# Performance work log

Measured on AMD Instinct MI355X. Metric: run time of the kernel, lower is better.

The kernel has to match this reference:

```python
import jax, jax.numpy as jnp
import numpy as np

B, N, D = 4, 1024, 1024
H = 16
DH = D // H  # 64
DROPOUT_P = 0.5


def setup_inputs() -> dict:
    key = jax.random.key(0)
    ks = jax.random.split(key, 6)
    query = jax.random.normal(ks[0], (B, N, D), dtype=jnp.float32)
    key_t = jax.random.normal(ks[1], (B, N, D), dtype=jnp.float32)
    value = jax.random.normal(ks[2], (B, N, D), dtype=jnp.float32)
    # torch Linear(D, 3D): weight [3D, D], bias [3D]
    W_qkv = jax.random.normal(ks[3], (3 * D, D), dtype=jnp.float32) * (1.0 / np.sqrt(D))
    b_qkv = jax.random.normal(ks[4], (3 * D,), dtype=jnp.float32) * 0.01
    # inverted dropout mask: keep_prob = 1 - p, kept entries scaled by 1/keep
    keep = 1.0 - DROPOUT_P
    drop_mask = (jax.random.uniform(ks[5], (B * H, N, N)) < keep).astype(jnp.float32) / keep
    return {"query": query, "key": key_t, "value": value,
            "W_qkv": W_qkv, "b_qkv": b_qkv, "drop_mask": drop_mask}


def _split_heads(t):
    # 'b n (h d) -> (b h) n d'
    b, n, _ = t.shape
    return t.reshape(b, n, H, DH).transpose(0, 2, 1, 3).reshape(b * H, n, DH)


def reference(query, key, value, W_qkv, b_qkv, drop_mask):
    # key/value args are unused by the original module (it derives q,k,v from query)
    qkv = query @ W_qkv.T + b_qkv                      # [b, n, 3d]
    q, k, v = jnp.split(qkv, 3, axis=-1)
    q, k, v = _split_heads(q), _split_heads(k), _split_heads(v)  # [(b h), n, dh]
    qk = jnp.einsum('znd,zmd->znm', q, k)              # [(b h), n, n]
    # faithful quirk: original does qk.div(1/sqrt(dh)) == qk * sqrt(dh)
    scaled_qk = qk * jnp.sqrt(jnp.float32(DH))
    attn = jax.nn.softmax(scaled_qk, axis=-1)
    attn = attn * drop_mask                            # deterministic inverted dropout
    out = jnp.einsum('znm,zmd->znd', attn, v)          # [(b h), n, dh]
    # '(b h) n d -> b n (h d)'
    out = out.reshape(B, H, N, DH).transpose(0, 2, 1, 3).reshape(B, N, D)
    return out
```

## Files before the change

kernel.cpp:

```cpp
#include <hip/hip_runtime.h>


typedef _Float16 f16;
typedef _Float16 f16x4 __attribute__((ext_vector_type(4)));
typedef _Float16 f16x8 __attribute__((ext_vector_type(8)));
typedef float    f32x4 __attribute__((ext_vector_type(4)));

#define MFMA16(a, b, c) __builtin_amdgcn_mfma_f32_16x16x32_f16((a), (b), (c), 0, 0, 0)

__device__ __forceinline__ void gll16(const f16* g, f16* l) {
  __builtin_amdgcn_global_load_lds(
      (const __attribute__((address_space(1))) unsigned int*)g,
      (__attribute__((address_space(3))) unsigned int*)l, 16, 0, 0);
}

__device__ __forceinline__ f16x8 ldsfrag(const f16* tile, int row, int chunk) {
  return *(const f16x8*)&tile[row * 64 + ((chunk ^ (row & 7)) << 3)];
}

__global__ __launch_bounds__(256) void cvt_split(const float4* __restrict__ s,
                                                 f16x4* __restrict__ hi,
                                                 f16x4* __restrict__ lo, int n4) {
  int i = blockIdx.x * 256 + threadIdx.x;
  if (i >= n4) return;
  float4 v = s[i];
  f16x4 h, l;
  h[0] = (f16)v.x; l[0] = (f16)(v.x - (float)h[0]);
  h[1] = (f16)v.y; l[1] = (f16)(v.y - (float)h[1]);
  h[2] = (f16)v.z; l[2] = (f16)(v.z - (float)h[2]);
  h[3] = (f16)v.w; l[3] = (f16)(v.w - (float)h[3]);
  hi[i] = h; lo[i] = l;
}

__global__ __launch_bounds__(256) void proj_gemm(
    const f16* __restrict__ qh, const f16* __restrict__ ql,
    const f16* __restrict__ wh, const f16* __restrict__ wl,
    const float* __restrict__ bias,
    f16* __restrict__ Qh, f16* __restrict__ Ql,
    f16* __restrict__ Kh, f16* __restrict__ Kl,
    f16* __restrict__ Vh) {
  __shared__ f16 As[128 * 32];
  __shared__ f16 Bs[128 * 32];
  const int tid = threadIdx.x;
  const int m0 = blockIdx.y * 128, n0 = blockIdx.x * 128;
  const int wid = tid >> 6, lane = tid & 63;
  const int wm = (wid >> 1) * 64, wn = (wid & 1) * 64;
  const int r16 = lane & 15, g = lane >> 4;

  f32x4 zero4 = {0.f, 0.f, 0.f, 0.f};
  f32x4 acc[4][4];
#pragma unroll
  for (int i = 0; i < 4; ++i)
#pragma unroll
    for (int j = 0; j < 4; ++j) acc[i][j] = zero4;

  const f16* At[3] = {qh, ql, qh};
  const f16* Bt[3] = {wh, wh, wl};
  const int nsteps = (n0 < 2048) ? 96 : 32;

  for (int s = 0; s < nsteps; ++s) {
    const int term = s >> 5, kk = (s & 31) << 5;
    const f16* Ab = At[term] + (size_t)m0 * 1024 + kk;
    const f16* Bb = Bt[term] + (size_t)n0 * 1024 + kk;
#pragma unroll
    for (int it = 0; it < 2; ++it) {
      int c = tid + it * 256;
      int row = c >> 2, cc = c & 3;
      gll16(Ab + row * 1024 + cc * 8, &As[c * 8]);
      gll16(Bb + row * 1024 + cc * 8, &Bs[c * 8]);
    }
    __syncthreads();
    f16x8 a[4], b[4];
#pragma unroll
    for (int i = 0; i < 4; ++i) {
      a[i] = *(const f16x8*)&As[(wm + i * 16 + r16) * 32 + g * 8];
      b[i] = *(const f16x8*)&Bs[(wn + i * 16 + r16) * 32 + g * 8];
    }
#pragma unroll
    for (int i = 0; i < 4; ++i)
#pragma unroll
      for (int j = 0; j < 4; ++j) acc[i][j] = MFMA16(a[i], b[j], acc[i][j]);
    __syncthreads();
  }

#pragma unroll
  for (int j = 0; j < 4; ++j) {
    const int col = n0 + wn + j * 16 + r16;
    const float bv = bias[col];
#pragma unroll
    for (int i = 0; i < 4; ++i) {
#pragma unroll
      for (int rr = 0; rr < 4; ++rr) {
        const int m = m0 + wm + i * 16 + g * 4 + rr;
        const float c = acc[i][j][rr] + bv;
        const int bi = m >> 10, n = m & 1023;
        if (col < 1024) {
          const int z = bi * 16 + (col >> 6), dh = col & 63;
          const size_t idx = ((size_t)z * 1024 + n) * 64 + dh;
          f16 h = (f16)c;
          Qh[idx] = h; Ql[idx] = (f16)(c - (float)h);
        } else if (col < 2048) {
          const int c2 = col - 1024;
          const int z = bi * 16 + (c2 >> 6), dh = c2 & 63;
          const size_t idx = ((size_t)z * 1024 + n) * 64 + dh;
          f16 h = (f16)c;
          Kh[idx] = h; Kl[idx] = (f16)(c - (float)h);
        } else {
          const int c2 = col - 2048;
          const int z = bi * 16 + (c2 >> 6), dh = c2 & 63;
          Vh[((size_t)z * 1024 + n) * 64 + dh] = (f16)c;
        }
      }
    }
  }
}

__global__ __launch_bounds__(256) void transp_v(const f16* __restrict__ Vh,
                                                f16* __restrict__ Vt) {
  __shared__ f16 t[64][80];
  const int z = blockIdx.y, nt = blockIdx.x;
  const int tid = threadIdx.x;
#pragma unroll
  for (int it = 0; it < 2; ++it) {
    int c = tid + it * 256;
    int row = c >> 3, cc = c & 7;
    *(f16x8*)&t[row][cc * 8] =
        *(const f16x8*)&Vh[(((size_t)z << 10) + nt * 64 + row) * 64 + cc * 8];
  }
  __syncthreads();
#pragma unroll
  for (int it = 0; it < 2; ++it) {
    int c = tid + it * 256;
    int dh = c >> 3, ncc = c & 7;
    f16x8 o;
#pragma unroll
    for (int j = 0; j < 8; ++j) o[j] = t[ncc * 8 + j][dh];
    *(f16x8*)&Vt[((size_t)z * 64 + dh) * 1024 + nt * 64 + ncc * 8] = o;
  }
}

__global__ __launch_bounds__(256) void attn(
    const f16* __restrict__ Qh_, const f16* __restrict__ Ql_,
    const f16* __restrict__ Kh_, const f16* __restrict__ Kl_,
    const f16* __restrict__ Vt_, const float* __restrict__ mask,
    float* __restrict__ out) {
  __shared__ f16 sm[5 * 4096];
  f16* Qhs = sm;
  f16* Qls = sm + 4096;
  f16* Khs = sm + 2 * 4096;
  f16* Kls = sm + 3 * 4096;
  f16* Vts = sm + 4 * 4096;
  f16* Ps = Khs;

  const int z = blockIdx.y, qt = blockIdx.x;
  const int q0 = qt * 64;
  const int tid = threadIdx.x, w = tid >> 6, lane = tid & 63;
  const int r16 = lane & 15, g = lane >> 4;

  const size_t qbase = ((size_t)z * 1024 + q0) * 64;
#pragma unroll
  for (int it = 0; it < 2; ++it) {
    int c = tid + it * 256;
    int row = c >> 3, p = c & 7, sc = p ^ (row & 7);
    gll16(Qh_ + qbase + row * 64 + sc * 8, &Qhs[c * 8]);
    gll16(Ql_ + qbase + row * 64 + sc * 8, &Qls[c * 8]);
  }
  __syncthreads();

  f16x8 qa[2], qla[2];
#pragma unroll
  for (int ks = 0; ks < 2; ++ks) {
    qa[ks] = ldsfrag(Qhs, w * 16 + r16, ks * 4 + g);
    qla[ks] = ldsfrag(Qls, w * 16 + r16, ks * 4 + g);
  }

  float mrow[4] = {-1e30f, -1e30f, -1e30f, -1e30f};
  float lrow[4] = {0.f, 0.f, 0.f, 0.f};
  f32x4 zero4 = {0.f, 0.f, 0.f, 0.f};
  f32x4 acc[4];
#pragma unroll
  for (int df = 0; df < 4; ++df) acc[df] = zero4;

  const float* mrow_base = mask + ((size_t)z << 20);

  for (int kt = 0; kt < 16; ++kt) {
    const int k0 = kt * 64;
    const size_t kbase = ((size_t)z * 1024 + k0) * 64;
    const size_t vbase = (size_t)z * 64 * 1024 + k0;
#pragma unroll
    for (int it = 0; it < 2; ++it) {
      int c = tid + it * 256;
      int row = c >> 3, p = c & 7, sc = p ^ (row & 7);
      gll16(Kh_ + kbase + row * 64 + sc * 8, &Khs[c * 8]);
      gll16(Kl_ + kbase + row * 64 + sc * 8, &Kls[c * 8]);
      gll16(Vt_ + vbase + (size_t)row * 1024 + sc * 8, &Vts[c * 8]);
    }
    __syncthreads();

    f32x4 s[4];
#pragma unroll
    for (int cf = 0; cf < 4; ++cf) {
      f32x4 t = zero4;
#pragma unroll
      for (int ks = 0; ks < 2; ++ks) {
        f16x8 kh = ldsfrag(Khs, cf * 16 + r16, ks * 4 + g);
        f16x8 kl = ldsfrag(Kls, cf * 16 + r16, ks * 4 + g);
        t = MFMA16(qa[ks], kh, t);
        t = MFMA16(qla[ks], kh, t);
        t = MFMA16(qa[ks], kl, t);
      }
      s[cf] = t;
    }

    float s8[4][4];
#pragma unroll
    for (int cf = 0; cf < 4; ++cf)
#pragma unroll
      for (int rr = 0; rr < 4; ++rr) s8[cf][rr] = s[cf][rr] * 8.0f;

    float rm[4];
#pragma unroll
    for (int rr = 0; rr < 4; ++rr)
      rm[rr] = fmaxf(fmaxf(s8[0][rr], s8[1][rr]), fmaxf(s8[2][rr], s8[3][rr]));
#pragma unroll
    for (int mk = 1; mk < 16; mk <<= 1)
#pragma unroll
      for (int rr = 0; rr < 4; ++rr)
        rm[rr] = fmaxf(rm[rr], __shfl_xor(rm[rr], mk, 64));

    float mnew[4], scal[4];
#pragma unroll
    for (int rr = 0; rr < 4; ++rr) {
      mnew[rr] = fmaxf(mrow[rr], rm[rr]);
      scal[rr] = __expf(mrow[rr] - mnew[rr]);
      mrow[rr] = mnew[rr];
    }

    float p_[4][4], rs[4] = {0.f, 0.f, 0.f, 0.f};
#pragma unroll
    for (int cf = 0; cf < 4; ++cf)
#pragma unroll
      for (int rr = 0; rr < 4; ++rr) {
        p_[cf][rr] = __expf(s8[cf][rr] - mnew[rr]);
        rs[rr] += p_[cf][rr];
      }
#pragma unroll
    for (int mk = 1; mk < 16; mk <<= 1)
#pragma unroll
      for (int rr = 0; rr < 4; ++rr) rs[rr] += __shfl_xor(rs[rr], mk, 64);
#pragma unroll
    for (int rr = 0; rr < 4; ++rr) lrow[rr] = lrow[rr] * scal[rr] + rs[rr];
#pragma unroll
    for (int df = 0; df < 4; ++df)
#pragma unroll
      for (int rr = 0; rr < 4; ++rr) acc[df][rr] *= scal[rr];

    float pm_[4][4];
#pragma unroll
    for (int cf = 0; cf < 4; ++cf)
#pragma unroll
      for (int rr = 0; rr < 4; ++rr) {
        const int qrow = q0 + w * 16 + g * 4 + rr;
        const float mv = mrow_base[(size_t)qrow * 1024 + k0 + cf * 16 + r16];
        pm_[cf][rr] = p_[cf][rr] * mv;
      }

    __syncthreads();

    f16* Pw = Ps + w * 1024;
#pragma unroll
    for (int cf = 0; cf < 4; ++cf)
#pragma unroll
      for (int rr = 0; rr < 4; ++rr) {
        const int prow = g * 4 + rr, key = cf * 16 + r16;
        Pw[prow * 64 + (((key >> 3) ^ (prow & 7)) << 3) + (key & 7)] =
            (f16)pm_[cf][rr];
      }
    f16x8 pf[2];
#pragma unroll
    for (int ks2 = 0; ks2 < 2; ++ks2) pf[ks2] = ldsfrag(Pw, r16, ks2 * 4 + g);
#pragma unroll
    for (int df = 0; df < 4; ++df)
#pragma unroll
      for (int ks2 = 0; ks2 < 2; ++ks2)
        acc[df] = MFMA16(pf[ks2], ldsfrag(Vts, df * 16 + r16, ks2 * 4 + g),
                         acc[df]);
    __syncthreads();
  }

  const int bi = z >> 4, hh = z & 15;
#pragma unroll
  for (int df = 0; df < 4; ++df)
#pragma unroll
    for (int rr = 0; rr < 4; ++rr) {
      const int n = q0 + w * 16 + g * 4 + rr;
      out[((size_t)bi * 1024 + n) * 1024 + hh * 64 + df * 16 + r16] =
          acc[df][rr] / lrow[rr];
    }
}

extern "C" void kernel_launch(void* const* d_in, const int* in_sizes, int n_in,
                              void* d_out, int out_size, void* d_ws,
                              size_t ws_size, hipStream_t stream) {
  const float* query = (const float*)d_in[0];
  const float* W = (const float*)d_in[3];
  const float* bias = (const float*)d_in[4];
  const float* mask = (const float*)d_in[5];
  float* out = (float*)d_out;

  f16* p = (f16*)d_ws;
  f16* qh = p;              p += (size_t)4096 * 1024;
  f16* ql = p;              p += (size_t)4096 * 1024;
  f16* wh = p;              p += (size_t)3072 * 1024;
  f16* wl = p;              p += (size_t)3072 * 1024;
  f16* Qh = p;              p += (size_t)64 * 1024 * 64;
  f16* Ql = p;              p += (size_t)64 * 1024 * 64;
  f16* Kh = p;              p += (size_t)64 * 1024 * 64;
  f16* Kl = p;              p += (size_t)64 * 1024 * 64;
  f16* Vh = p;              p += (size_t)64 * 1024 * 64;
  f16* Vt = p;

  cvt_split<<<(1048576 + 255) / 256, 256, 0, stream>>>(
      (const float4*)query, (f16x4*)qh, (f16x4*)ql, 1048576);
  cvt_split<<<(786432 + 255) / 256, 256, 0, stream>>>(
      (const float4*)W, (f16x4*)wh, (f16x4*)wl, 786432);
  proj_gemm<<<dim3(24, 32), 256, 0, stream>>>(qh, ql, wh, wl, bias, Qh, Ql, Kh,
                                              Kl, Vh);
  transp_v<<<dim3(16, 64), 256, 0, stream>>>(Vh, Vt);
  attn<<<dim3(16, 64), 256, 0, stream>>>(Qh, Ql, Kh, Kl, Vt, mask, out);
}
```

Baseline: 538.3 us.

## Load attention K/V/Q fragments directly from global, drop shared-memory staging

The attention kernel no longer stages Q, K and V tiles in shared memory via global_load_lds. Each wave instead loads its MFMA operand fragments straight from global memory and keeps only a small per-wave P buffer in LDS. This removes both block-wide __syncthreads per key tile and lets the dropout mask loads be issued earlier. The cost is redundant global/L2 traffic, since all four waves reload the same K/V fragments, and the loads become less coalesced.

After: 648.9 us. 1.21x slower.

```diff
diff --git a/kernel.cpp b/kernel.cpp
--- a/kernel.cpp
+++ b/kernel.cpp
@@ -12,10 +12,6 @@
   __builtin_amdgcn_global_load_lds(
       (const __attribute__((address_space(1))) unsigned int*)g,
       (__attribute__((address_space(3))) unsigned int*)l, 16, 0, 0);
-}
-
-__device__ __forceinline__ f16x8 ldsfrag(const f16* tile, int row, int chunk) {
-  return *(const f16x8*)&tile[row * 64 + ((chunk ^ (row & 7)) << 3)];
 }
 
 __global__ __launch_bounds__(256) void cvt_split(const float4* __restrict__ s,
@@ -144,35 +140,27 @@
     const f16* __restrict__ Kh_, const f16* __restrict__ Kl_,
     const f16* __restrict__ Vt_, const float* __restrict__ mask,
     float* __restrict__ out) {
-  __shared__ f16 sm[5 * 4096];
-  f16* Qhs = sm;
-  f16* Qls = sm + 4096;
-  f16* Khs = sm + 2 * 4096;
-  f16* Kls = sm + 3 * 4096;
-  f16* Vts = sm + 4 * 4096;
-  f16* Ps = Khs;
+  __shared__ f16 Ps[4][1024];
 
   const int z = blockIdx.y, qt = blockIdx.x;
   const int q0 = qt * 64;
   const int tid = threadIdx.x, w = tid >> 6, lane = tid & 63;
   const int r16 = lane & 15, g = lane >> 4;
 
-  const size_t qbase = ((size_t)z * 1024 + q0) * 64;
-#pragma unroll
-  for (int it = 0; it < 2; ++it) {
-    int c = tid + it * 256;
-    int row = c >> 3, p = c & 7, sc = p ^ (row & 7);
-    gll16(Qh_ + qbase + row * 64 + sc * 8, &Qhs[c * 8]);
-    gll16(Ql_ + qbase + row * 64 + sc * 8, &Qls[c * 8]);
-  }
-  __syncthreads();
-
+  const f16* qrh = Qh_ + ((size_t)z * 1024 + q0 + w * 16 + r16) * 64;
+  const f16* qrl = Ql_ + ((size_t)z * 1024 + q0 + w * 16 + r16) * 64;
   f16x8 qa[2], qla[2];
 #pragma unroll
   for (int ks = 0; ks < 2; ++ks) {
-    qa[ks] = ldsfrag(Qhs, w * 16 + r16, ks * 4 + g);
-    qla[ks] = ldsfrag(Qls, w * 16 + r16, ks * 4 + g);
-  }
+    qa[ks] = *(const f16x8*)&qrh[ks * 32 + g * 8];
+    qla[ks] = *(const f16x8*)&qrl[ks * 32 + g * 8];
+  }
+
+  const f16* Kzh = Kh_ + ((size_t)z << 10) * 64;
+  const f16* Kzl = Kl_ + ((size_t)z << 10) * 64;
+  const f16* Vz = Vt_ + (size_t)z * 64 * 1024;
+  const float* mz = mask + ((size_t)z << 20);
+  const int qrow_m = q0 + w * 16 + g * 4;
 
   float mrow[4] = {-1e30f, -1e30f, -1e30f, -1e30f};
   float lrow[4] = {0.f, 0.f, 0.f, 0.f};
@@ -181,34 +169,34 @@
 #pragma unroll
   for (int df = 0; df < 4; ++df) acc[df] = zero4;
 
-  const float* mrow_base = mask + ((size_t)z << 20);
+  f16* Pw = &Ps[w][0];
 
   for (int kt = 0; kt < 16; ++kt) {
     const int k0 = kt * 64;
-    const size_t kbase = ((size_t)z * 1024 + k0) * 64;
-    const size_t vbase = (size_t)z * 64 * 1024 + k0;
-#pragma unroll
-    for (int it = 0; it < 2; ++it) {
-      int c = tid + it * 256;
-      int row = c >> 3, p = c & 7, sc = p ^ (row & 7);
-      gll16(Kh_ + kbase + row * 64 + sc * 8, &Khs[c * 8]);
-      gll16(Kl_ + kbase + row * 64 + sc * 8, &Kls[c * 8]);
-      gll16(Vt_ + vbase + (size_t)row * 1024 + sc * 8, &Vts[c * 8]);
-    }
-    __syncthreads();
+
+    float mv[4][4];
+#pragma unroll
+    for (int cf = 0; cf < 4; ++cf)
+#pragma unroll
+      for (int rr = 0; rr < 4; ++rr)
+        mv[cf][rr] = mz[(size_t)(qrow_m + rr) * 1024 + k0 + cf * 16 + r16];
 
     f32x4 s[4];
 #pragma unroll
     for (int cf = 0; cf < 4; ++cf) {
+      const f16* kb = Kzh + (size_t)(k0 + cf * 16 + r16) * 64;
+      const f16* klb = Kzl + (size_t)(k0 + cf * 16 + r16) * 64;
+      f16x8 kh0 = *(const f16x8*)&kb[g * 8];
+      f16x8 kh1 = *(const f16x8*)&kb[32 + g * 8];
+      f16x8 kl0 = *(const f16x8*)&klb[g * 8];
+      f16x8 kl1 = *(const f16x8*)&klb[32 + g * 8];
       f32x4 t = zero4;
-#pragma unroll
-      for (int ks = 0; ks < 2; ++ks) {
-        f16x8 kh = ldsfrag(Khs, cf * 16 + r16, ks * 4 + g);
-        f16x8 kl = ldsfrag(Kls, cf * 16 + r16, ks * 4 + g);
-        t = MFMA16(qa[ks], kh, t);
-        t = MFMA16(qla[ks], kh, t);
-        t = MFMA16(qa[ks], kl, t);
-      }
+      t = MFMA16(qa[0], kh0, t);
+      t = MFMA16(qla[0], kh0, t);
+      t = MFMA16(qa[0], kl0, t);
+      t = MFMA16(qa[1], kh1, t);
+      t = MFMA16(qla[1], kh1, t);
+      t = MFMA16(qa[1], kl1, t);
       s[cf] = t;
     }
 
@@ -255,37 +243,29 @@
 #pragma unroll
       for (int rr = 0; rr < 4; ++rr) acc[df][rr] *= scal[rr];
 
-    float pm_[4][4];
-#pragma unroll
-    for (int cf = 0; cf < 4; ++cf)
-#pragma unroll
-      for (int rr = 0; rr < 4; ++rr) {
-        const int qrow = q0 + w * 16 + g * 4 + rr;
-        const float mv = mrow_base[(size_t)qrow * 1024 + k0 + cf * 16 + r16];
-        pm_[cf][rr] = p_[cf][rr] * mv;
-      }
-
-    __syncthreads();
-
-    f16* Pw = Ps + w * 1024;
 #pragma unroll
     for (int cf = 0; cf < 4; ++cf)
 #pragma unroll
       for (int rr = 0; rr < 4; ++rr) {
         const int prow = g * 4 + rr, key = cf * 16 + r16;
         Pw[prow * 64 + (((key >> 3) ^ (prow & 7)) << 3) + (key & 7)] =
-            (f16)pm_[cf][rr];
+            (f16)(p_[cf][rr] * mv[cf][rr]);
       }
     f16x8 pf[2];
 #pragma unroll
-    for (int ks2 = 0; ks2 < 2; ++ks2) pf[ks2] = ldsfrag(Pw, r16, ks2 * 4 + g);
-#pragma unroll
-    for (int df = 0; df < 4; ++df)
+    for (int ks2 = 0; ks2 < 2; ++ks2) {
+      const int row = r16, c = ks2 * 4 + g;
+      pf[ks2] = *(const f16x8*)&Pw[row * 64 + ((c ^ (row & 7)) << 3)];
+    }
+
+#pragma unroll
+    for (int df = 0; df < 4; ++df) {
+      const f16* vb = Vz + (size_t)(df * 16 + r16) * 1024 + k0;
 #pragma unroll
       for (int ks2 = 0; ks2 < 2; ++ks2)
-        acc[df] = MFMA16(pf[ks2], ldsfrag(Vts, df * 16 + r16, ks2 * 4 + g),
-                         acc[df]);
-    __syncthreads();
+        acc[df] =
+            MFMA16(pf[ks2], *(const f16x8*)&vb[ks2 * 32 + g * 8], acc[df]);
+    }
   }
 
   const int bi = z >> 4, hh = z & 15;
```
